# Kernel tuning notes

Hardware: AMD Instinct MI355X
Metric: run time of the kernel (lower is better)

Reference implementation:

```python
import jax, jax.numpy as jnp
import numpy as np

B, TQ, TK, QD, KD = 16, 256, 256, 512, 512

def setup_inputs() -> dict:
    key = jax.random.key(0)
    k = jax.random.split(key, 8)
    query = jax.random.normal(k[0], (B, TQ, QD), dtype=jnp.float32)
    keys = jax.random.normal(k[1], (B, TK, KD), dtype=jnp.float32)
    # linear_q: query_size -> key_size (stored as [in, out] for x @ W)
    Wq = jax.random.normal(k[2], (QD, KD), dtype=jnp.float32) * 0.02
    bq = jnp.zeros((KD,), dtype=jnp.float32)
    # linear_att: key_size -> 1
    w_att = jax.random.normal(k[3], (KD,), dtype=jnp.float32) * 0.02
    b_att = jnp.zeros((), dtype=jnp.float32)
    # linear_out: (query_size + key_size) -> query_size
    Wout = jax.random.normal(k[4], (QD + KD, QD), dtype=jnp.float32) * 0.02
    bout = jnp.zeros((QD,), dtype=jnp.float32)
    return {"query": query, "keys": keys, "Wq": Wq, "bq": bq,
            "w_att": w_att, "b_att": b_att, "Wout": Wout, "bout": bout}

def reference(query, keys, Wq, bq, w_att, b_att, Wout, bout):
    # att_query = linear_q(query): [b, t_q, n]
    att_query = query @ Wq + bq
    # Bahdanau additive score: tanh(q_i + k_j) . w + b  -> [b, t_q, t_k]
    sum_qk = jnp.tanh(att_query[:, :, None, :] + keys[:, None, :, :])  # b,tq,tk,n
    scores = jnp.einsum('bqkn,n->bqk', sum_qk, w_att) + b_att
    p = jax.nn.softmax(scores, axis=-1)  # softmax over t_k
    # values defaults to keys
    context = jnp.einsum('bqk,bkn->bqn', p, keys)
    # output transform: tanh(linear_out([query; context]))
    context = jnp.tanh(jnp.concatenate([query, context], axis=-1) @ Wout + bout)
    return context, p
```

## Files before the change

### kernel.cpp

```cpp
#include <hip/hip_runtime.h>


#define C2 2.88539008177792681f

typedef unsigned short u16;
typedef short s16x8 __attribute__((ext_vector_type(8)));
typedef float f32x4 __attribute__((ext_vector_type(4)));
typedef float f32x2 __attribute__((ext_vector_type(2)));

__device__ __forceinline__ float fast_rcp(float x) { return __builtin_amdgcn_rcpf(x); }
__device__ __forceinline__ f32x2 fma2(f32x2 a, f32x2 b, f32x2 c) {
  return __builtin_elementwise_fma(a, b, c);
}

__device__ __forceinline__ u16 f2bf(float f) {
  union { float f; unsigned u; } v; v.f = f;
  unsigned r = v.u + 0x7fffu + ((v.u >> 16) & 1u);
  return (u16)(r >> 16);
}
__device__ __forceinline__ unsigned packbf(float a, float b) {
  return (unsigned)f2bf(a) | ((unsigned)f2bf(b) << 16);
}

__global__ __launch_bounds__(256) void mega_prep(
    const float* __restrict__ keys, float* __restrict__ Ek,
    const float* __restrict__ query, u16* __restrict__ qbf,
    u16* __restrict__ kbfT,
    const float* __restrict__ Wq, u16* __restrict__ Wqt,
    const float* __restrict__ Wout, u16* __restrict__ Woutt,
    const float* __restrict__ w_att, const float* __restrict__ b_att,
    float* __restrict__ Cptr)
{
  __shared__ float red[4];
  __shared__ u16 tile[32][40];
  const int t = threadIdx.x;
  const int bx = blockIdx.x;

  if (bx < 2048) {
    const size_t i4 = (size_t)bx * 256 + t;
    float4 v = ((const float4*)keys)[i4];
    float4 o;
    o.x = exp2f(C2 * v.x); o.y = exp2f(C2 * v.y);
    o.z = exp2f(C2 * v.z); o.w = exp2f(C2 * v.w);
    ((float4*)Ek)[i4] = o;
    if (bx == 0) {
      float wsum = w_att[t] + w_att[t + 256];
#pragma unroll
      for (int m = 32; m; m >>= 1) wsum += __shfl_xor(wsum, m);
      if ((t & 63) == 0) red[t >> 6] = wsum;
      __syncthreads();
      if (t == 0) Cptr[0] = red[0] + red[1] + red[2] + red[3] + b_att[0];
    }
  } else if (bx < 3072) {
    const size_t i8 = ((size_t)(bx - 2048) * 256 + t) * 8;
    float4 a = *(const float4*)&query[i8];
    float4 b = *(const float4*)&query[i8 + 4];
    unsigned p0 = packbf(a.x, a.y), p1 = packbf(a.z, a.w);
    unsigned p2 = packbf(b.x, b.y), p3 = packbf(b.z, b.w);
    *(int4*)&qbf[i8] = make_int4(p0, p1, p2, p3);
  } else if (bx < 5120) {
    const int b2 = bx - 3072;
    const int n0 = (b2 & 15) * 32, k0 = ((b2 >> 4) & 7) * 32, b = b2 >> 7;
    const float* src = keys + (size_t)b * 131072;
    u16* dst = kbfT + (size_t)b * 131072;
    const int r = t >> 3, c = (t & 7) * 4;
    float4 v = *(const float4*)&src[(size_t)(k0 + r) * 512 + n0 + c];
    tile[c + 0][r] = f2bf(v.x); tile[c + 1][r] = f2bf(v.y);
    tile[c + 2][r] = f2bf(v.z); tile[c + 3][r] = f2bf(v.w);
    __syncthreads();
    if (t < 128) {
      const int row = t >> 2, ch = (t & 3) * 8;
      unsigned p0 = (unsigned)tile[row][ch + 0] | ((unsigned)tile[row][ch + 1] << 16);
      unsigned p1 = (unsigned)tile[row][ch + 2] | ((unsigned)tile[row][ch + 3] << 16);
      unsigned p2 = (unsigned)tile[row][ch + 4] | ((unsigned)tile[row][ch + 5] << 16);
      unsigned p3 = (unsigned)tile[row][ch + 6] | ((unsigned)tile[row][ch + 7] << 16);
      *(int4*)&dst[(size_t)(n0 + row) * 256 + k0 + ch] = make_int4(p0, p1, p2, p3);
    }
  } else {
    const int b3 = bx - 5120;
    const int by = b3 >> 4;
    const int n0 = (b3 & 15) * 32;
    const float* W; u16* Wt; int K, k0;
    if (by < 16) { W = Wq;   Wt = Wqt;   K = 512;  k0 = by * 32; }
    else         { W = Wout; Wt = Woutt; K = 1024; k0 = (by - 16) * 32; }
    const int r = t >> 3, c = (t & 7) * 4;
    float4 v = *(const float4*)&W[(size_t)(k0 + r) * 512 + n0 + c];
    tile[c + 0][r] = f2bf(v.x); tile[c + 1][r] = f2bf(v.y);
    tile[c + 2][r] = f2bf(v.z); tile[c + 3][r] = f2bf(v.w);
    __syncthreads();
    if (t < 128) {
      const int row = t >> 2, ch = (t & 3) * 8;
      unsigned p0 = (unsigned)tile[row][ch + 0] | ((unsigned)tile[row][ch + 1] << 16);
      unsigned p1 = (unsigned)tile[row][ch + 2] | ((unsigned)tile[row][ch + 3] << 16);
      unsigned p2 = (unsigned)tile[row][ch + 4] | ((unsigned)tile[row][ch + 5] << 16);
      unsigned p3 = (unsigned)tile[row][ch + 6] | ((unsigned)tile[row][ch + 7] << 16);
      *(int4*)&Wt[(size_t)(n0 + row) * K + k0 + ch] = make_int4(p0, p1, p2, p3);
    }
  }
}

__global__ __launch_bounds__(256) void gemm_mfma_bf16(
    const u16* __restrict__ A0, const u16* __restrict__ A1, int kSplit,
    const u16* __restrict__ Bt, const float* __restrict__ bias,
    float* __restrict__ C, int K, int act)
{
  __shared__ u16 As[64 * 72];
  __shared__ u16 Bs[64 * 72];
  const int t = threadIdx.x;
  const int lane = t & 63, wid = t >> 6;
  const int wm = wid >> 1, wn = wid & 1;
  const int col0 = blockIdx.x * 64, row0 = blockIdx.y * 64;
  const int lr = t >> 2, lc = (t & 3) * 16;
  const int fr = lane & 15, fg = (lane >> 4) * 8;

  f32x4 acc[2][2] = {};
  const int nIter = K >> 6;

  int4 a0v, a1v, b0v, b1v;
  {
    const u16* Asrc = (0 < kSplit) ? A0 : A1;
    a0v = *(const int4*)&Asrc[(size_t)(row0 + lr) * 512 + lc];
    a1v = *(const int4*)&Asrc[(size_t)(row0 + lr) * 512 + lc + 8];
    b0v = *(const int4*)&Bt[(size_t)(col0 + lr) * K + lc];
    b1v = *(const int4*)&Bt[(size_t)(col0 + lr) * K + lc + 8];
  }
  for (int it = 0; it < nIter; ++it) {
    __syncthreads();
    *(int4*)&As[lr * 72 + lc]     = a0v;
    *(int4*)&As[lr * 72 + lc + 8] = a1v;
    *(int4*)&Bs[lr * 72 + lc]     = b0v;
    *(int4*)&Bs[lr * 72 + lc + 8] = b1v;
    __syncthreads();

    if (it + 1 < nIter) {
      const int k0 = (it + 1) << 6;
      const u16* Asrc; int kc;
      if (k0 < kSplit) { Asrc = A0; kc = k0; } else { Asrc = A1; kc = k0 - kSplit; }
      a0v = *(const int4*)&Asrc[(size_t)(row0 + lr) * 512 + kc + lc];
      a1v = *(const int4*)&Asrc[(size_t)(row0 + lr) * 512 + kc + lc + 8];
      b0v = *(const int4*)&Bt[(size_t)(col0 + lr) * K + k0 + lc];
      b1v = *(const int4*)&Bt[(size_t)(col0 + lr) * K + k0 + lc + 8];
    }

#pragma unroll
    for (int ks = 0; ks < 2; ++ks) {
      s16x8 af[2], bf[2];
#pragma unroll
      for (int m = 0; m < 2; ++m)
        af[m] = *(const s16x8*)&As[(wm * 32 + m * 16 + fr) * 72 + ks * 32 + fg];
#pragma unroll
      for (int n = 0; n < 2; ++n)
        bf[n] = *(const s16x8*)&Bs[(wn * 32 + n * 16 + fr) * 72 + ks * 32 + fg];
#pragma unroll
      for (int m = 0; m < 2; ++m)
#pragma unroll
        for (int n = 0; n < 2; ++n)
          acc[m][n] = __builtin_amdgcn_mfma_f32_16x16x32_bf16(af[m], bf[n], acc[m][n], 0, 0, 0);
    }
  }

  const int fq = lane >> 4;
#pragma unroll
  for (int n = 0; n < 2; ++n) {
    const int col = col0 + wn * 32 + n * 16 + fr;
    const float bv = bias[col];
#pragma unroll
    for (int m = 0; m < 2; ++m) {
#pragma unroll
      for (int i = 0; i < 4; ++i) {
        const int row = row0 + wm * 32 + m * 16 + fq * 4 + i;
        float v = acc[m][n][i] + bv;
        if (act == 1) {
          float e = __expf(2.0f * v);
          v = 1.0f - 2.0f * fast_rcp(e + 1.0f);
        } else if (act == 2) {
          v = exp2f(C2 * v);
        }
        C[(size_t)row * 512 + col] = v;
      }
    }
  }
}

__global__ __launch_bounds__(256) void score_kernel(
    const float* __restrict__ Ea, const float* __restrict__ Ek,
    const float* __restrict__ w_att, const float* __restrict__ Cptr,
    float* __restrict__ S)
{
  __shared__ float ea_s[64][68];
  __shared__ float ek_s[64][68];

  const int z = blockIdx.z;
  const int b = z >> 2, qt = z & 3;
  const int q0 = blockIdx.y * 64, k0 = blockIdx.x * 64;
  const int t = threadIdx.x;

  const int qi = t >> 4, ki = t & 15;
  const int lr = t >> 2, lc = (t & 3) * 16;
  const float* eap = Ea + (size_t)(b * 256 + q0) * 512 + qt * 128;
  const float* ekp = Ek + (size_t)(b * 256 + k0) * 512 + qt * 128;
  const float* wbase = w_att + qt * 128;

  float acc[4][4] = {};
  const f32x2 one = {1.0f, 1.0f};

  for (int c = 0; c < 2; ++c) {
    const int gb = lr * 512 + c * 64 + lc;
    float4 A0 = *(const float4*)&eap[gb + 0];
    float4 A1 = *(const float4*)&eap[gb + 4];
    float4 A2 = *(const float4*)&eap[gb + 8];
    float4 A3 = *(const float4*)&eap[gb + 12];
    float4 K0 = *(const float4*)&ekp[gb + 0];
    float4 K1 = *(const float4*)&ekp[gb + 4];
    float4 K2 = *(const float4*)&ekp[gb + 8];
    float4 K3 = *(const float4*)&ekp[gb + 12];
    __syncthreads();
    *(float4*)&ea_s[lr][lc + 0]  = A0;
    *(float4*)&ea_s[lr][lc + 4]  = A1;
    *(float4*)&ea_s[lr][lc + 8]  = A2;
    *(float4*)&ea_s[lr][lc + 12] = A3;
    *(float4*)&ek_s[lr][lc + 0]  = K0;
    *(float4*)&ek_s[lr][lc + 4]  = K1;
    *(float4*)&ek_s[lr][lc + 8]  = K2;
    *(float4*)&ek_s[lr][lc + 12] = K3;
    __syncthreads();

    for (int j = 0; j < 64; j += 8) {
      f32x2 kp[4][4];
#pragma unroll
      for (int n = 0; n < 4; ++n) {
        float4 kv0 = *(const float4*)&ek_s[ki + n * 16][j];
        float4 kv1 = *(const float4*)&ek_s[ki + n * 16][j + 4];
        kp[n][0] = f32x2{kv0.x, kv0.y};
        kp[n][1] = f32x2{kv0.z, kv0.w};
        kp[n][2] = f32x2{kv1.x, kv1.y};
        kp[n][3] = f32x2{kv1.z, kv1.w};
      }
      const float* wq = wbase + c * 64 + j;
      f32x2 wp0 = {wq[0], wq[1]};
      f32x2 wp1 = {wq[2], wq[3]};
      f32x2 wp2 = {wq[4], wq[5]};
      f32x2 wp3 = {wq[6], wq[7]};

#pragma unroll
      for (int m = 0; m < 4; ++m) {
        float4 av0 = *(const float4*)&ea_s[qi + m * 16][j];
        float4 av1 = *(const float4*)&ea_s[qi + m * 16][j + 4];
        f32x2 ap0 = {av0.x, av0.y};
        f32x2 ap1 = {av0.z, av0.w};
        f32x2 ap2 = {av1.x, av1.y};
        f32x2 ap3 = {av1.z, av1.w};
#pragma unroll
        for (int n = 0; n < 4; ++n) {
          f32x2 q1 = fma2(ap0, kp[n][0], one);
          f32x2 q2 = fma2(ap1, kp[n][1], one);
          f32x2 q3 = fma2(ap2, kp[n][2], one);
          f32x2 q4 = fma2(ap3, kp[n][3], one);
          f32x2 N12 = fma2(wp0, q2, wp1 * q1);
          f32x2 D12 = q1 * q2;
          f32x2 N34 = fma2(wp2, q4, wp3 * q3);
          f32x2 D34 = q3 * q4;
          f32x2 Nt = fma2(N12, D34, N34 * D12);
          f32x2 Dt = D12 * D34;
          float r0 = fast_rcp(Dt.x);
          float r1 = fast_rcp(Dt.y);
          acc[m][n] = fmaf(Nt.x, r0, acc[m][n]);
          acc[m][n] = fmaf(Nt.y, r1, acc[m][n]);
        }
      }
    }
  }

  const float Cv = (qt == 0) ? Cptr[0] : 0.0f;
  float* sc = S + (size_t)qt * 1048576;
#pragma unroll
  for (int m = 0; m < 4; ++m) {
    const size_t qr = (size_t)(b * 256 + q0 + qi + m * 16);
#pragma unroll
    for (int n = 0; n < 4; ++n)
      sc[qr * 256 + k0 + ki + n * 16] = fmaf(-2.f, acc[m][n], Cv);
  }
}

__global__ __launch_bounds__(256) void softmax_kernel(
    const float* __restrict__ S, float* __restrict__ p_out,
    u16* __restrict__ pbf)
{
  const int t = threadIdx.x;
  const int w = t >> 6, lane = t & 63;
  const int row = blockIdx.x * 4 + w;
  const size_t off = (size_t)row * 256 + lane * 4;
  float4 sa = *(const float4*)&S[off];
  float4 sb = *(const float4*)&S[off + 1048576];
  float4 sc = *(const float4*)&S[off + 2097152];
  float4 sd = *(const float4*)&S[off + 3145728];
  float4 s4 = {(sa.x + sb.x) + (sc.x + sd.x), (sa.y + sb.y) + (sc.y + sd.y),
               (sa.z + sb.z) + (sc.z + sd.z), (sa.w + sb.w) + (sc.w + sd.w)};
  float m = fmaxf(fmaxf(s4.x, s4.y), fmaxf(s4.z, s4.w));
#pragma unroll
  for (int msk = 32; msk; msk >>= 1) m = fmaxf(m, __shfl_xor(m, msk));
  float e0 = __expf(s4.x - m);
  float e1 = __expf(s4.y - m);
  float e2 = __expf(s4.z - m);
  float e3 = __expf(s4.w - m);
  float ssum = (e0 + e1) + (e2 + e3);
#pragma unroll
  for (int msk = 32; msk; msk >>= 1) ssum += __shfl_xor(ssum, msk);
  float rs = 1.0f / ssum;
  float4 p4 = {e0 * rs, e1 * rs, e2 * rs, e3 * rs};
  *(float4*)&p_out[off] = p4;
  unsigned lo = packbf(p4.x, p4.y), hi = packbf(p4.z, p4.w);
  *(int2*)&pbf[off] = make_int2(lo, hi);
}

__global__ __launch_bounds__(256) void ctx_gemm(
    const u16* __restrict__ pbf, const u16* __restrict__ kbfT,
    u16* __restrict__ ctxbf)
{
  __shared__ u16 As[64 * 72];
  __shared__ u16 Bs[64 * 72];
  const int t = threadIdx.x;
  const int lane = t & 63, wid = t >> 6;
  const int wm = wid >> 1, wn = wid & 1;
  const int col0 = blockIdx.x * 64, row0 = blockIdx.y * 64, b = blockIdx.z;
  const u16* A = pbf + (size_t)b * 65536;
  const u16* Bm = kbfT + (size_t)b * 131072;
  const int lr = t >> 2, lc = (t & 3) * 16;
  const int fr = lane & 15, fg = (lane >> 4) * 8;

  f32x4 acc[2][2] = {};

  int4 a0v = *(const int4*)&A[(size_t)(row0 + lr) * 256 + lc];
  int4 a1v = *(const int4*)&A[(size_t)(row0 + lr) * 256 + lc + 8];
  int4 b0v = *(const int4*)&Bm[(size_t)(col0 + lr) * 256 + lc];
  int4 b1v = *(const int4*)&Bm[(size_t)(col0 + lr) * 256 + lc + 8];

  for (int it = 0; it < 4; ++it) {
    __syncthreads();
    *(int4*)&As[lr * 72 + lc]     = a0v;
    *(int4*)&As[lr * 72 + lc + 8] = a1v;
    *(int4*)&Bs[lr * 72 + lc]     = b0v;
    *(int4*)&Bs[lr * 72 + lc + 8] = b1v;
    __syncthreads();

    if (it < 3) {
      const int k0 = (it + 1) << 6;
      a0v = *(const int4*)&A[(size_t)(row0 + lr) * 256 + k0 + lc];
      a1v = *(const int4*)&A[(size_t)(row0 + lr) * 256 + k0 + lc + 8];
      b0v = *(const int4*)&Bm[(size_t)(col0 + lr) * 256 + k0 + lc];
      b1v = *(const int4*)&Bm[(size_t)(col0 + lr) * 256 + k0 + lc + 8];
    }

#pragma unroll
    for (int ks = 0; ks < 2; ++ks) {
      s16x8 af[2], bf[2];
#pragma unroll
      for (int m = 0; m < 2; ++m)
        af[m] = *(const s16x8*)&As[(wm * 32 + m * 16 + fr) * 72 + ks * 32 + fg];
#pragma unroll
      for (int n = 0; n < 2; ++n)
        bf[n] = *(const s16x8*)&Bs[(wn * 32 + n * 16 + fr) * 72 + ks * 32 + fg];
#pragma unroll
      for (int m = 0; m < 2; ++m)
#pragma unroll
        for (int n = 0; n < 2; ++n)
          acc[m][n] = __builtin_amdgcn_mfma_f32_16x16x32_bf16(af[m], bf[n], acc[m][n], 0, 0, 0);
    }
  }

  const int fq = lane >> 4;
#pragma unroll
  for (int n = 0; n < 2; ++n) {
    const int col = col0 + wn * 32 + n * 16 + fr;
#pragma unroll
    for (int m = 0; m < 2; ++m) {
#pragma unroll
      for (int i = 0; i < 4; ++i) {
        const int row = row0 + wm * 32 + m * 16 + fq * 4 + i;
        ctxbf[(size_t)(b * 256 + row) * 512 + col] = f2bf(acc[m][n][i]);
      }
    }
  }
}

extern "C" void kernel_launch(void* const* d_in, const int* in_sizes, int n_in,
                              void* d_out, int out_size, void* d_ws, size_t ws_size,
                              hipStream_t stream) {
  const float* query = (const float*)d_in[0];
  const float* keys  = (const float*)d_in[1];
  const float* Wq    = (const float*)d_in[2];
  const float* bq    = (const float*)d_in[3];
  const float* w_att = (const float*)d_in[4];
  const float* b_att = (const float*)d_in[5];
  const float* Wout  = (const float*)d_in[6];
  const float* bout  = (const float*)d_in[7];

  float* out_tanh = (float*)d_out;
  float* out_p    = out_tanh + (size_t)4096 * 512;

  float* ws = (float*)d_ws;
  float* Ea     = ws;
  float* Ek     = ws + 2097152;
  float* S      = ws + 4194304;
  float* Cptr   = ws + 8388608;
  u16*   Wqt    = (u16*)(ws + 8388624);
  u16*   Woutt  = Wqt + 262144;
  u16*   qbf    = Woutt + 524288;
  u16*   kbfT   = qbf + 2097152;
  u16*   pbf    = kbfT + 2097152;
  u16*   ctxbf  = (u16*)Ea;

  mega_prep<<<5888, 256, 0, stream>>>(
      keys, Ek, query, qbf, kbfT, Wq, Wqt, Wout, Woutt, w_att, b_att, Cptr);

  gemm_mfma_bf16<<<dim3(8, 64), 256, 0, stream>>>(
      qbf, qbf, 512, Wqt, bq, Ea, 512, 2);

  score_kernel<<<dim3(4, 4, 64), 256, 0, stream>>>(
      Ea, Ek, w_att, Cptr, S);

  softmax_kernel<<<1024, 256, 0, stream>>>(S, out_p, pbf);

  ctx_gemm<<<dim3(8, 4, 16), 256, 0, stream>>>(pbf, kbfT, ctxbf);

  gemm_mfma_bf16<<<dim3(8, 64), 256, 0, stream>>>(
      qbf, ctxbf, 512, Woutt, bout, out_tanh, 1024, 1);
}
```

Baseline: 101.0 us.

## Fuse keys exp and bf16 transpose in prep; widen GEMM K-tile to 128

The prep kernel now reads each keys tile once and writes both the exp-transformed Ek and the transposed bf16 kbfT from the same load. The separate transpose blocks are gone and the w_att reduction moves to its own final block, so the grid shrinks from 5888 to 3841 blocks and keys are read from global memory half as often. The bf16 MFMA GEMM also doubles its K step per iteration to 128, with larger shared tiles and four 16-byte loads per thread, which halves the number of barrier-separated iterations. The cost is more shared memory and more registers held per thread in the GEMM, and fewer blocks when the keys tile is written as Ek, which changes that write pattern.

After: 145.8 us. 44.4% more time.

```diff
diff --git a/kernel.cpp b/kernel.cpp
--- a/kernel.cpp
+++ b/kernel.cpp
@@ -37,19 +37,27 @@
   const int bx = blockIdx.x;
 
   if (bx < 2048) {
-    const size_t i4 = (size_t)bx * 256 + t;
-    float4 v = ((const float4*)keys)[i4];
+    const int b = bx >> 7, rem = bx & 127;
+    const int k0 = (rem >> 4) * 32, n0 = (rem & 15) * 32;
+    const float* src = keys + (size_t)b * 131072;
+    const int r = t >> 3, c = (t & 7) * 4;
+    const size_t off = (size_t)(k0 + r) * 512 + n0 + c;
+    float4 v = *(const float4*)&src[off];
     float4 o;
     o.x = exp2f(C2 * v.x); o.y = exp2f(C2 * v.y);
     o.z = exp2f(C2 * v.z); o.w = exp2f(C2 * v.w);
-    ((float4*)Ek)[i4] = o;
-    if (bx == 0) {
-      float wsum = w_att[t] + w_att[t + 256];
-#pragma unroll
-      for (int m = 32; m; m >>= 1) wsum += __shfl_xor(wsum, m);
-      if ((t & 63) == 0) red[t >> 6] = wsum;
-      __syncthreads();
-      if (t == 0) Cptr[0] = red[0] + red[1] + red[2] + red[3] + b_att[0];
+    *(float4*)&Ek[(size_t)b * 131072 + off] = o;
+    tile[c + 0][r] = f2bf(v.x); tile[c + 1][r] = f2bf(v.y);
+    tile[c + 2][r] = f2bf(v.z); tile[c + 3][r] = f2bf(v.w);
+    __syncthreads();
+    if (t < 128) {
+      const int row = t >> 2, ch = (t & 3) * 8;
+      unsigned p0 = (unsigned)tile[row][ch + 0] | ((unsigned)tile[row][ch + 1] << 16);
+      unsigned p1 = (unsigned)tile[row][ch + 2] | ((unsigned)tile[row][ch + 3] << 16);
+      unsigned p2 = (unsigned)tile[row][ch + 4] | ((unsigned)tile[row][ch + 5] << 16);
+      unsigned p3 = (unsigned)tile[row][ch + 6] | ((unsigned)tile[row][ch + 7] << 16);
+      *(int4*)&kbfT[(size_t)b * 131072 + (size_t)(n0 + row) * 256 + k0 + ch] =
+          make_int4(p0, p1, p2, p3);
     }
   } else if (bx < 3072) {
     const size_t i8 = ((size_t)(bx - 2048) * 256 + t) * 8;
@@ -58,26 +66,8 @@
     unsigned p0 = packbf(a.x, a.y), p1 = packbf(a.z, a.w);
     unsigned p2 = packbf(b.x, b.y), p3 = packbf(b.z, b.w);
     *(int4*)&qbf[i8] = make_int4(p0, p1, p2, p3);
-  } else if (bx < 5120) {
-    const int b2 = bx - 3072;
-    const int n0 = (b2 & 15) * 32, k0 = ((b2 >> 4) & 7) * 32, b = b2 >> 7;
-    const float* src = keys + (size_t)b * 131072;
-    u16* dst = kbfT + (size_t)b * 131072;
-    const int r = t >> 3, c = (t & 7) * 4;
-    float4 v = *(const float4*)&src[(size_t)(k0 + r) * 512 + n0 + c];
-    tile[c + 0][r] = f2bf(v.x); tile[c + 1][r] = f2bf(v.y);
-    tile[c + 2][r] = f2bf(v.z); tile[c + 3][r] = f2bf(v.w);
-    __syncthreads();
-    if (t < 128) {
-      const int row = t >> 2, ch = (t & 3) * 8;
-      unsigned p0 = (unsigned)tile[row][ch + 0] | ((unsigned)tile[row][ch + 1] << 16);
-      unsigned p1 = (unsigned)tile[row][ch + 2] | ((unsigned)tile[row][ch + 3] << 16);
-      unsigned p2 = (unsigned)tile[row][ch + 4] | ((unsigned)tile[row][ch + 5] << 16);
-      unsigned p3 = (unsigned)tile[row][ch + 6] | ((unsigned)tile[row][ch + 7] << 16);
-      *(int4*)&dst[(size_t)(n0 + row) * 256 + k0 + ch] = make_int4(p0, p1, p2, p3);
-    }
-  } else {
-    const int b3 = bx - 5120;
+  } else if (bx < 3840) {
+    const int b3 = bx - 3072;
     const int by = b3 >> 4;
     const int n0 = (b3 & 15) * 32;
     const float* W; u16* Wt; int K, k0;
@@ -96,6 +86,13 @@
       unsigned p3 = (unsigned)tile[row][ch + 6] | ((unsigned)tile[row][ch + 7] << 16);
       *(int4*)&Wt[(size_t)(n0 + row) * K + k0 + ch] = make_int4(p0, p1, p2, p3);
     }
+  } else {
+    float wsum = w_att[t] + w_att[t + 256];
+#pragma unroll
+    for (int m = 32; m; m >>= 1) wsum += __shfl_xor(wsum, m);
+    if ((t & 63) == 0) red[t >> 6] = wsum;
+    __syncthreads();
+    if (t == 0) Cptr[0] = red[0] + red[1] + red[2] + red[3] + b_att[0];
   }
 }
 
@@ -104,53 +101,60 @@
     const u16* __restrict__ Bt, const float* __restrict__ bias,
     float* __restrict__ C, int K, int act)
 {
-  __shared__ u16 As[64 * 72];
-  __shared__ u16 Bs[64 * 72];
+  __shared__ u16 As[64 * 136];
+  __shared__ u16 Bs[64 * 136];
   const int t = threadIdx.x;
   const int lane = t & 63, wid = t >> 6;
   const int wm = wid >> 1, wn = wid & 1;
   const int col0 = blockIdx.x * 64, row0 = blockIdx.y * 64;
-  const int lr = t >> 2, lc = (t & 3) * 16;
+  const int lr = t >> 2, lc = (t & 3) * 32;
   const int fr = lane & 15, fg = (lane >> 4) * 8;
 
   f32x4 acc[2][2] = {};
-  const int nIter = K >> 6;
-
-  int4 a0v, a1v, b0v, b1v;
+  const int nIter = K >> 7;
+
+  int4 av[4], bv[4];
   {
     const u16* Asrc = (0 < kSplit) ? A0 : A1;
-    a0v = *(const int4*)&Asrc[(size_t)(row0 + lr) * 512 + lc];
-    a1v = *(const int4*)&Asrc[(size_t)(row0 + lr) * 512 + lc + 8];
-    b0v = *(const int4*)&Bt[(size_t)(col0 + lr) * K + lc];
-    b1v = *(const int4*)&Bt[(size_t)(col0 + lr) * K + lc + 8];
+    const u16* ap = &Asrc[(size_t)(row0 + lr) * 512 + lc];
+    const u16* bp = &Bt[(size_t)(col0 + lr) * K + lc];
+#pragma unroll
+    for (int u = 0; u < 4; ++u) {
+      av[u] = *(const int4*)(ap + u * 8);
+      bv[u] = *(const int4*)(bp + u * 8);
+    }
   }
   for (int it = 0; it < nIter; ++it) {
     __syncthreads();
-    *(int4*)&As[lr * 72 + lc]     = a0v;
-    *(int4*)&As[lr * 72 + lc + 8] = a1v;
-    *(int4*)&Bs[lr * 72 + lc]     = b0v;
-    *(int4*)&Bs[lr * 72 + lc + 8] = b1v;
+#pragma unroll
+    for (int u = 0; u < 4; ++u) {
+      *(int4*)&As[lr * 136 + lc + u * 8] = av[u];
+      *(int4*)&Bs[lr * 136 + lc + u * 8] = bv[u];
+    }
     __syncthreads();
 
     if (it + 1 < nIter) {
-      const int k0 = (it + 1) << 6;
+      const int k0 = (it + 1) << 7;
       const u16* Asrc; int kc;
       if (k0 < kSplit) { Asrc = A0; kc = k0; } else { Asrc = A1; kc = k0 - kSplit; }
-      a0v = *(const int4*)&Asrc[(size_t)(row0 + lr) * 512 + kc + lc];
-      a1v = *(const int4*)&Asrc[(size_t)(row0 + lr) * 512 + kc + lc + 8];
-      b0v = *(const int4*)&Bt[(size_t)(col0 + lr) * K + k0 + lc];
-      b1v = *(const int4*)&Bt[(size_t)(col0 + lr) * K + k0 + lc + 8];
-    }
-
-#pragma unroll
-    for (int ks = 0; ks < 2; ++ks) {
+      const u16* ap = &Asrc[(size_t)(row0 + lr) * 512 + kc + lc];
+      const u16* bp = &Bt[(size_t)(col0 + lr) * K + k0 + lc];
+#pragma unroll
+      for (int u = 0; u < 4; ++u) {
+        av[u] = *(const int4*)(ap + u * 8);
+        bv[u] = *(const int4*)(bp + u * 8);
+      }
+    }
+
+#pragma unroll
+    for (int ks = 0; ks < 4; ++ks) {
       s16x8 af[2], bf[2];
 #pragma unroll
       for (int m = 0; m < 2; ++m)
-        af[m] = *(const s16x8*)&As[(wm * 32 + m * 16 + fr) * 72 + ks * 32 + fg];
+        af[m] = *(const s16x8*)&As[(wm * 32 + m * 16 + fr) * 136 + ks * 32 + fg];
 #pragma unroll
       for (int n = 0; n < 2; ++n)
-        bf[n] = *(const s16x8*)&Bs[(wn * 32 + n * 16 + fr) * 72 + ks * 32 + fg];
+        bf[n] = *(const s16x8*)&Bs[(wn * 32 + n * 16 + fr) * 136 + ks * 32 + fg];
 #pragma unroll
       for (int m = 0; m < 2; ++m)
 #pragma unroll
@@ -163,13 +167,13 @@
 #pragma unroll
   for (int n = 0; n < 2; ++n) {
     const int col = col0 + wn * 32 + n * 16 + fr;
-    const float bv = bias[col];
+    const float bv2 = bias[col];
 #pragma unroll
     for (int m = 0; m < 2; ++m) {
 #pragma unroll
       for (int i = 0; i < 4; ++i) {
         const int row = row0 + wm * 32 + m * 16 + fq * 4 + i;
-        float v = acc[m][n][i] + bv;
+        float v = acc[m][n][i] + bv2;
         if (act == 1) {
           float e = __expf(2.0f * v);
           v = 1.0f - 2.0f * fast_rcp(e + 1.0f);
@@ -410,7 +414,7 @@
   u16*   pbf    = kbfT + 2097152;
   u16*   ctxbf  = (u16*)Ea;
 
-  mega_prep<<<5888, 256, 0, stream>>>(
+  mega_prep<<<3841, 256, 0, stream>>>(
       keys, Ek, query, qbf, kbfT, Wq, Wqt, Wout, Woutt, w_att, b_att, Cptr);
 
   gemm_mfma_bf16<<<dim3(8, 64), 256, 0, stream>>>(
```
